# Kernel tuning notes

Hardware: AMD Instinct MI355X
Metric: run time of the kernel (lower is better)

The kernel has to match this reference:

```python
import jax, jax.numpy as jnp
import numpy as np

B, C, H, W = 32, 256, 64, 64
MIP, HID, OUT = 8, 256, 14  # mip = max(8, 256//32); per_eye=7 -> 2*7=14
MIN_Z, MAX_Z = 0.5, 1000.0


def _hswish(x):
    return x * jnp.clip(x + 3.0, 0.0, 6.0) / 6.0


def _bn(x, g, b, m, v, axis, eps=1e-5):
    sh = [1] * x.ndim
    sh[axis] = -1
    return (x - m.reshape(sh)) * (g.reshape(sh) / jnp.sqrt(v.reshape(sh) + eps)) + b.reshape(sh)


def _safe_norm(v, axis=-1, eps=1e-8):
    return v / (jnp.linalg.norm(v, axis=axis, keepdims=True) + eps)


def setup_inputs() -> dict:
    key = jax.random.key(0)
    ks = jax.random.split(key, 8)
    x = jax.random.normal(ks[0], (B, C, H, W), dtype=jnp.float32)
    K1 = jnp.array([[500.0, 0.0, 320.0], [0.0, 500.0, 240.0], [0.0, 0.0, 1.0]], jnp.float32)
    K = jnp.tile(K1[None], (B, 1, 1))
    iris_radius_cm = 0.6 * jnp.ones((B,), jnp.float32)
    s = 0.05
    return {
        'x': x, 'K': K, 'iris_radius_cm': iris_radius_cm,
        'ca_w1': s * jax.random.normal(ks[1], (MIP, C), jnp.float32),
        'ca_bn_g': jnp.ones((MIP,), jnp.float32), 'ca_bn_b': jnp.zeros((MIP,), jnp.float32),
        'ca_bn_m': jnp.zeros((MIP,), jnp.float32), 'ca_bn_v': jnp.ones((MIP,), jnp.float32),
        'ca_wh': s * jax.random.normal(ks[2], (C, MIP), jnp.float32),
        'ca_ww': s * jax.random.normal(ks[3], (C, MIP), jnp.float32),
        'fc1_w': s * jax.random.normal(ks[4], (HID, C), jnp.float32),
        'fc1_b': jnp.zeros((HID,), jnp.float32),
        'bn1_g': jnp.ones((HID,), jnp.float32), 'bn1_b': jnp.zeros((HID,), jnp.float32),
        'bn1_m': jnp.zeros((HID,), jnp.float32), 'bn1_v': jnp.ones((HID,), jnp.float32),
        'fc_out_w': s * jax.random.normal(ks[5], (OUT, HID), jnp.float32),
        'fc_out_b': jnp.zeros((OUT,), jnp.float32),
    }


def _forward(x, K, iris_radius_cm, ca_w1, ca_bn_g, ca_bn_b, ca_bn_m, ca_bn_v,
             ca_wh, ca_ww, fc1_w, fc1_b, bn1_g, bn1_b, bn1_m, bn1_v, fc_out_w, fc_out_b):
    b, c, h, w = x.shape
    # ---- CoordAtt ----
    xh = x.mean(axis=3)                      # [B,C,H]
    xw = x.mean(axis=2)                      # [B,C,W]
    y = jnp.concatenate([xh, xw], axis=2)    # [B,C,H+W]
    y = jnp.einsum('mc,bcl->bml', ca_w1, y)  # 1x1 conv -> [B,mip,H+W]
    y = _hswish(_bn(y, ca_bn_g, ca_bn_b, ca_bn_m, ca_bn_v, axis=1))
    a_h = jax.nn.sigmoid(jnp.einsum('cm,bmh->bch', ca_wh, y[:, :, :h]))[:, :, :, None]
    a_w = jax.nn.sigmoid(jnp.einsum('cm,bmw->bcw', ca_ww, y[:, :, h:]))[:, :, None, :]
    x = x * a_h * a_w
    # ---- pool + MLP head ----
    p = x.mean(axis=(2, 3))                                  # [B,C]
    hdd = jnp.maximum(_bn(p @ fc1_w.T + fc1_b, bn1_g, bn1_b, bn1_m, bn1_v, axis=1), 0.0)
    raw = hdd @ fc_out_w.T + fc_out_b                        # [B,14]
    t = raw.reshape(b, 2, 7)                                 # eyes L,R
    # ---- unpack per-eye ellipse ----
    cx, cy = t[..., 0], t[..., 1]
    ea = jax.nn.softplus(t[..., 2]) + 1e-6
    eb = jax.nn.softplus(t[..., 3]) + 1e-6
    ang = _safe_norm(t[..., 4:6])
    cth, sth = ang[..., 0], ang[..., 1]
    delta_cm = 0.3 * jnp.tanh(t[..., 6:7])                   # [B,2,1]
    ellipse = jnp.stack([cx, cy, ea, eb, cth, sth], axis=-1) # [B,2,6]
    # ---- ellipse -> conic C (pixel), then Cn = K^T C K ----
    theta = jnp.arctan2(sth, cth)
    ct, st = jnp.cos(theta), jnp.sin(theta)
    ia2, ib2 = 1.0 / (ea * ea), 1.0 / (eb * eb)
    A11 = ct * ct * ia2 + st * st * ib2
    A22 = st * st * ia2 + ct * ct * ib2
    A12 = ct * st * (ia2 - ib2)
    ax = A11 * cx + A12 * cy
    ay = A12 * cx + A22 * cy
    cAc = A11 * cx ** 2 + 2.0 * A12 * cx * cy + A22 * cy ** 2
    Cm = jnp.stack([jnp.stack([A11, A12, -ax], -1),
                    jnp.stack([A12, A22, -ay], -1),
                    jnp.stack([-ax, -ay, cAc - 1.0], -1)], -2)  # [B,2,3,3]
    Cn = jnp.einsum('bji,bejk,bkl->beil', K, Cm, K)             # [B,2,3,3]
    # ---- 2x2 solve + eigh on normalized conic ----
    A = Cn[..., :2, :2]
    u = Cn[..., :2, 2]
    mu = jnp.linalg.solve(A, -u[..., None])[..., 0]             # [B,2,2]
    evals, evecs = jnp.linalg.eigh(A)                           # ascending
    a_n = 1.0 / jnp.sqrt(jnp.maximum(evals[..., 0], 1e-12))
    b_n = 1.0 / jnp.sqrt(jnp.maximum(evals[..., 1], 1e-12))
    v = evecs[..., :, 0]
    theta_n = jnp.arctan2(v[..., 1], v[..., 0])                 # [B,2]
    # ---- lift to 3D pose + center ----
    a_n = jnp.maximum(a_n, 1e-6)
    R = iris_radius_cm[:, None]
    z = jnp.clip(R / a_n, MIN_Z, MAX_Z)[..., None]              # [B,2,1]
    ray = _safe_norm(jnp.stack([mu[..., 0], mu[..., 1], jnp.ones_like(mu[..., 0])], -1))
    iris_center = ray * z                                       # [B,2,3]
    tilt = jnp.arccos(jnp.clip(b_n / a_n, 0.0, 1.0))[..., None] # [B,2,1]
    axis3 = jnp.stack([jnp.cos(theta_n), jnp.sin(theta_n), jnp.zeros_like(theta_n)], -1)
    k = _safe_norm(axis3)
    z_ax = jnp.broadcast_to(jnp.array([0.0, 0.0, 1.0], x.dtype), k.shape)
    ctl, stl = jnp.cos(tilt), jnp.sin(tilt)
    kv = jnp.cross(k, z_ax)
    kdv = jnp.sum(k * z_ax, -1, keepdims=True)
    normal = _safe_norm(z_ax * ctl + kv * stl + k * (kdv * (1.0 - ctl)))
    pupil_center = iris_center + delta_cm * normal
    return ellipse, delta_cm, iris_center, normal, pupil_center, z


def reference(x, K, iris_radius_cm, ca_w1, ca_bn_g, ca_bn_b, ca_bn_m, ca_bn_v,
              ca_wh, ca_ww, fc1_w, fc1_b, bn1_g, bn1_b, bn1_m, bn1_v, fc_out_w, fc_out_b):
    return _forward(x, K, iris_radius_cm, ca_w1, ca_bn_g, ca_bn_b, ca_bn_m, ca_bn_v,
                    ca_wh, ca_ww, fc1_w, fc1_b, bn1_g, bn1_b, bn1_m, bn1_v, fc_out_w, fc_out_b)
```

## Files before the change

kernel.cpp:

```cpp
#include <hip/hip_runtime.h>
#include <math.h>

#define Bb 32
#define Cc 256
#define Hh 64
#define Ww 64
#define MIP 8
#define HID 256
#define NOUT 14

__global__ __launch_bounds__(256) void k1_sums(const float* __restrict__ x,
                                               float* __restrict__ S) {
    const int bc = blockIdx.x;
    const float4* xp = (const float4*)(x + (size_t)bc * (Hh * Ww));
    const int t = threadIdx.x;
    const int cw = t & 15;
    const int rb = t >> 4;
    __shared__ float rowpart[64][17];
    __shared__ float colpart[16][64];
    float4 v[4];
#pragma unroll
    for (int k = 0; k < 4; ++k) v[k] = xp[t + 256 * k];
    float c0 = 0.f, c1 = 0.f, c2 = 0.f, c3 = 0.f;
#pragma unroll
    for (int k = 0; k < 4; ++k) {
        rowpart[rb + 16 * k][cw] = v[k].x + v[k].y + v[k].z + v[k].w;
        c0 += v[k].x; c1 += v[k].y; c2 += v[k].z; c3 += v[k].w;
    }
    colpart[rb][cw * 4 + 0] = c0;
    colpart[rb][cw * 4 + 1] = c1;
    colpart[rb][cw * 4 + 2] = c2;
    colpart[rb][cw * 4 + 3] = c3;
    __syncthreads();
    float* out = S + (size_t)bc * 128;
    if (t < 64) {
        float s = 0.f;
#pragma unroll
        for (int i = 0; i < 16; ++i) s += rowpart[t][i];
        out[t] = s;
    } else if (t < 128) {
        const int w = t - 64;
        float s = 0.f;
#pragma unroll
        for (int g = 0; g < 16; ++g) s += colpart[g][w];
        out[64 + w] = s;
    }
}

__global__ __launch_bounds__(256) void k2_yact(const float* __restrict__ S,
                                               const float* __restrict__ w1,
                                               const float* __restrict__ bng,
                                               const float* __restrict__ bnb,
                                               const float* __restrict__ bnm,
                                               const float* __restrict__ bnv,
                                               float* __restrict__ yact) {
    const int b = blockIdx.x;
    const int t = threadIdx.x;
    const int half = __builtin_amdgcn_readfirstlane(t >> 7);
    const int l = t & 127;
    __shared__ float part[2][MIP][128];
    const float* Sp = S + (size_t)b * Cc * 128 + (size_t)half * 128 * 128 + l;
    const float* wp = w1 + half * 128;
    float a0 = 0.f, a1 = 0.f, a2 = 0.f, a3 = 0.f,
          a4 = 0.f, a5 = 0.f, a6 = 0.f, a7 = 0.f;
#pragma unroll 4
    for (int cc = 0; cc < 128; ++cc) {
        float s = Sp[(size_t)cc * 128];
        a0 += wp[0 * Cc + cc] * s;
        a1 += wp[1 * Cc + cc] * s;
        a2 += wp[2 * Cc + cc] * s;
        a3 += wp[3 * Cc + cc] * s;
        a4 += wp[4 * Cc + cc] * s;
        a5 += wp[5 * Cc + cc] * s;
        a6 += wp[6 * Cc + cc] * s;
        a7 += wp[7 * Cc + cc] * s;
    }
    part[half][0][l] = a0; part[half][1][l] = a1;
    part[half][2][l] = a2; part[half][3][l] = a3;
    part[half][4][l] = a4; part[half][5][l] = a5;
    part[half][6][l] = a6; part[half][7][l] = a7;
    __syncthreads();
    if (t < 128) {
#pragma unroll
        for (int m = 0; m < MIP; ++m) {
            float sum = (part[0][m][l] + part[1][m][l]) * (1.0f / 64.0f);
            float y = (sum - bnm[m]) * (bng[m] / sqrtf(bnv[m] + 1e-5f)) + bnb[m];
            float cl = fminf(fmaxf(y + 3.0f, 0.0f), 6.0f);
            yact[((size_t)b * MIP + m) * 128 + l] = y * cl * (1.0f / 6.0f);
        }
    }
}

__global__ __launch_bounds__(256) void k3_pool(const float* __restrict__ x,
                                               const float* __restrict__ yact,
                                               const float* __restrict__ wh,
                                               const float* __restrict__ ww,
                                               float* __restrict__ p) {
    const int bc = blockIdx.x;
    const int b = bc >> 8;
    const int c = bc & 255;
    const int t = threadIdx.x;
    __shared__ float ah[64], aw[64], red[4];
    if (t < 128) {
        const float* yb = yact + (size_t)b * MIP * 128;
        const float* wv = (t < 64) ? (wh + c * MIP) : (ww + c * MIP);
        float acc = 0.f;
#pragma unroll
        for (int m = 0; m < MIP; ++m) acc += wv[m] * yb[m * 128 + t];
        float s = 1.0f / (1.0f + expf(-acc));
        if (t < 64) ah[t] = s; else aw[t - 64] = s;
    }
    __syncthreads();
    const float4* xp = (const float4*)(x + (size_t)bc * (Hh * Ww));
    const int cw = t & 15, rb = t >> 4;
    float partial = 0.f;
#pragma unroll
    for (int k = 0; k < 4; ++k) {
        float4 v = xp[t + 256 * k];
        float rd = v.x * aw[cw * 4 + 0] + v.y * aw[cw * 4 + 1] +
                   v.z * aw[cw * 4 + 2] + v.w * aw[cw * 4 + 3];
        partial += ah[rb + 16 * k] * rd;
    }
#pragma unroll
    for (int off = 32; off > 0; off >>= 1) partial += __shfl_down(partial, off, 64);
    if ((t & 63) == 0) red[t >> 6] = partial;
    __syncthreads();
    if (t == 0) p[bc] = (red[0] + red[1] + red[2] + red[3]) * (1.0f / (float)(Hh * Ww));
}

__device__ inline double softplus_d(double xx) {
    return fmax(xx, 0.0) + log1p(exp(-fabs(xx)));
}

__global__ __launch_bounds__(256) void k4_head(
    const float* __restrict__ p,
    const float* __restrict__ fc1_w, const float* __restrict__ fc1_b,
    const float* __restrict__ bn1_g, const float* __restrict__ bn1_b,
    const float* __restrict__ bn1_m, const float* __restrict__ bn1_v,
    const float* __restrict__ fo_w, const float* __restrict__ fo_b,
    const float* __restrict__ Kmat, const float* __restrict__ iris_r,
    float* __restrict__ out) {
    const int b = blockIdx.x, t = threadIdx.x;
    __shared__ float pl[256], hdd[256], raw[16];
    __shared__ float part2[NOUT][16];
    pl[t] = p[b * 256 + t];
    __syncthreads();
    const float4* wrow = (const float4*)(fc1_w + (size_t)t * 256);
    float acc = fc1_b[t];
#pragma unroll 4
    for (int c4 = 0; c4 < 64; ++c4) {
        float4 w4 = wrow[c4];
        acc += w4.x * pl[c4 * 4] + w4.y * pl[c4 * 4 + 1] +
               w4.z * pl[c4 * 4 + 2] + w4.w * pl[c4 * 4 + 3];
    }
    float ybn = (acc - bn1_m[t]) * (bn1_g[t] / sqrtf(bn1_v[t] + 1e-5f)) + bn1_b[t];
    hdd[t] = fmaxf(ybn, 0.f);
    __syncthreads();
    if (t < NOUT * 16) {
        const int o = t >> 4, lane16 = t & 15;
        const float* wo = fo_w + o * HID + lane16;
        float a = 0.f;
#pragma unroll
        for (int j = 0; j < 16; ++j) a += wo[j * 16] * hdd[lane16 + j * 16];
        part2[o][lane16] = a;
    }
    __syncthreads();
    if (t < NOUT) {
        float a = fo_b[t];
#pragma unroll
        for (int i = 0; i < 16; ++i) a += part2[t][i];
        raw[t] = a;
    }
    __syncthreads();
    if (t < 2) {
        const int e = t;
        const float* tv = raw + e * 7;
        double t0 = tv[0], t1 = tv[1], t2 = tv[2], t3 = tv[3],
               t4 = tv[4], t5 = tv[5], t6 = tv[6];
        double cx = t0, cy = t1;
        double ea = softplus_d(t2) + 1e-6;
        double eb = softplus_d(t3) + 1e-6;
        double rr = sqrt(t4 * t4 + t5 * t5) + 1e-8;
        double cth = t4 / rr, sth = t5 / rr;
        double delta = 0.3 * tanh(t6);
        const int be = b * 2 + e;
        out[be * 6 + 0] = (float)cx;
        out[be * 6 + 1] = (float)cy;
        out[be * 6 + 2] = (float)ea;
        out[be * 6 + 3] = (float)eb;
        out[be * 6 + 4] = (float)cth;
        out[be * 6 + 5] = (float)sth;
        out[384 + be] = (float)delta;

        double ct = cth, st = sth;
        double ia2 = 1.0 / (ea * ea), ib2 = 1.0 / (eb * eb);
        double A11 = ct * ct * ia2 + st * st * ib2;
        double A22 = st * st * ia2 + ct * ct * ib2;
        double A12 = ct * st * (ia2 - ib2);
        double axp = A11 * cx + A12 * cy;
        double ayp = A12 * cx + A22 * cy;
        double cAc = A11 * cx * cx + 2.0 * A12 * cx * cy + A22 * cy * cy;
        double Cm[3][3] = {{A11, A12, -axp}, {A12, A22, -ayp}, {-axp, -ayp, cAc - 1.0}};
        double Kd[3][3];
        for (int i = 0; i < 3; ++i)
            for (int j = 0; j < 3; ++j) Kd[i][j] = (double)Kmat[b * 9 + i * 3 + j];
        double M[3][3], Cn[3][3];
        for (int j = 0; j < 3; ++j)
            for (int l = 0; l < 3; ++l) {
                double s = 0.0;
                for (int k = 0; k < 3; ++k) s += Cm[j][k] * Kd[k][l];
                M[j][l] = s;
            }
        for (int i = 0; i < 3; ++i)
            for (int l = 0; l < 3; ++l) {
                double s = 0.0;
                for (int j = 0; j < 3; ++j) s += Kd[j][i] * M[j][l];
                Cn[i][l] = s;
            }
        double Aa = Cn[0][0], Ab = Cn[1][0], Ac = Cn[1][1];
        double A01 = Cn[0][1];
        double u0 = Cn[0][2], u1 = Cn[1][2];
        double det = Aa * Ac - A01 * Ab;
        double mux = (A01 * u1 - Ac * u0) / det;
        double muy = (Ab * u0 - Aa * u1) / det;
        double sm = Aa + Ac, df = Aa - Ac;
        double adf = fabs(df);
        double tb = Ab + Ab, ab = fabs(tb);
        double acmx, acmn;
        if (fabs(Aa) > fabs(Ac)) { acmx = Aa; acmn = Ac; } else { acmx = Ac; acmn = Aa; }
        double rt;
        if (adf > ab)      rt = adf * sqrt(1.0 + (ab / adf) * (ab / adf));
        else if (adf < ab) rt = ab * sqrt(1.0 + (adf / ab) * (adf / ab));
        else               rt = ab * sqrt(2.0);
        double rt1, rt2; int sgn1;
        if (sm < 0.0)      { rt1 = 0.5 * (sm - rt); sgn1 = -1;
                             rt2 = (acmx / rt1) * acmn - (Ab / rt1) * Ab; }
        else if (sm > 0.0) { rt1 = 0.5 * (sm + rt); sgn1 = 1;
                             rt2 = (acmx / rt1) * acmn - (Ab / rt1) * Ab; }
        else               { rt1 = 0.5 * rt; rt2 = -0.5 * rt; sgn1 = 1; }
        double cs; int sgn2;
        if (df >= 0.0) { cs = df + rt; sgn2 = 1; } else { cs = df - rt; sgn2 = -1; }
        double acs = fabs(cs), cs1, sn1;
        if (acs > ab) {
            double ctv = -tb / cs;
            sn1 = 1.0 / sqrt(1.0 + ctv * ctv);
            cs1 = ctv * sn1;
        } else if (ab == 0.0) {
            cs1 = 1.0; sn1 = 0.0;
        } else {
            double tn = -cs / tb;
            cs1 = 1.0 / sqrt(1.0 + tn * tn);
            sn1 = tn * cs1;
        }
        if (sgn1 == sgn2) { double tmp = cs1; cs1 = -sn1; sn1 = tmp; }
        double lam0, lam1, vx, vy;
        if (rt2 < rt1) { lam0 = rt2; lam1 = rt1; vx = -sn1; vy = cs1; }
        else           { lam0 = rt1; lam1 = rt2; vx = cs1;  vy = sn1; }
        double a_n = 1.0 / sqrt(fmax(lam0, 1e-12));
        double b_n = 1.0 / sqrt(fmax(lam1, 1e-12));
        a_n = fmax(a_n, 1e-6);
        double Rir = (double)iris_r[b];
        double zz = fmin(fmax(Rir / a_n, 0.5), 1000.0);
        double rnorm = sqrt(mux * mux + muy * muy + 1.0) + 1e-8;
        double ic0 = (mux / rnorm) * zz, ic1 = (muy / rnorm) * zz, ic2 = (1.0 / rnorm) * zz;
        double a3x = vx, a3y = vy;
        double kn = sqrt(a3x * a3x + a3y * a3y) + 1e-8;
        double kx = a3x / kn, ky = a3y / kn;
        double rba = fmin(fmax(b_n / a_n, 0.0), 1.0);
        double ctl = rba, stl = sqrt(fmax(1.0 - rba * rba, 0.0));
        double nx = ky * stl, ny = -kx * stl, nz = ctl;
        double nn = sqrt(nx * nx + ny * ny + nz * nz) + 1e-8;
        nx /= nn; ny /= nn; nz /= nn;
        out[448 + be * 3 + 0] = (float)ic0;
        out[448 + be * 3 + 1] = (float)ic1;
        out[448 + be * 3 + 2] = (float)ic2;
        out[640 + be * 3 + 0] = (float)nx;
        out[640 + be * 3 + 1] = (float)ny;
        out[640 + be * 3 + 2] = (float)nz;
        out[832 + be * 3 + 0] = (float)(ic0 + delta * nx);
        out[832 + be * 3 + 1] = (float)(ic1 + delta * ny);
        out[832 + be * 3 + 2] = (float)(ic2 + delta * nz);
        out[1024 + be] = (float)zz;
    }
}

extern "C" void kernel_launch(void* const* d_in, const int* in_sizes, int n_in,
                              void* d_out, int out_size, void* d_ws, size_t ws_size,
                              hipStream_t stream) {
    const float* x     = (const float*)d_in[0];
    const float* Kmat  = (const float*)d_in[1];
    const float* iris  = (const float*)d_in[2];
    const float* ca_w1 = (const float*)d_in[3];
    const float* ca_g  = (const float*)d_in[4];
    const float* ca_b  = (const float*)d_in[5];
    const float* ca_m  = (const float*)d_in[6];
    const float* ca_v  = (const float*)d_in[7];
    const float* ca_wh = (const float*)d_in[8];
    const float* ca_ww = (const float*)d_in[9];
    const float* fc1_w = (const float*)d_in[10];
    const float* fc1_b = (const float*)d_in[11];
    const float* bn1_g = (const float*)d_in[12];
    const float* bn1_b = (const float*)d_in[13];
    const float* bn1_m = (const float*)d_in[14];
    const float* bn1_v = (const float*)d_in[15];
    const float* fo_w  = (const float*)d_in[16];
    const float* fo_b  = (const float*)d_in[17];

    float* ws   = (float*)d_ws;
    float* S    = ws;
    float* yact = S + (size_t)Bb * Cc * 128;
    float* p    = yact + (size_t)Bb * MIP * 128;

    k1_sums<<<Bb * Cc, 256, 0, stream>>>(x, S);
    k2_yact<<<Bb, 256, 0, stream>>>(S, ca_w1, ca_g, ca_b, ca_m, ca_v, yact);
    k3_pool<<<Bb * Cc, 256, 0, stream>>>(x, yact, ca_wh, ca_ww, p);
    k4_head<<<Bb, 256, 0, stream>>>(p, fc1_w, fc1_b, bn1_g, bn1_b, bn1_m, bn1_v,
                                    fo_w, fo_b, Kmat, iris, (float*)d_out);
}
```

Measured before the change: 267.8 us.

## Fuse per-batch reductions into producer kernels via last-block atomic counters

```diff
diff --git a/kernel.cpp b/kernel.cpp
--- a/kernel.cpp
+++ b/kernel.cpp
@@ -9,98 +9,120 @@
 #define HID 256
 #define NOUT 14
 
-__global__ __launch_bounds__(256) void k1_sums(const float* __restrict__ x,
-                                               float* __restrict__ S) {
+__global__ __launch_bounds__(256) void kA_sums_yact(
+    const float* __restrict__ x, float* __restrict__ S,
+    const float* __restrict__ w1,
+    const float* __restrict__ bng, const float* __restrict__ bnb,
+    const float* __restrict__ bnm, const float* __restrict__ bnv,
+    float* __restrict__ yact, unsigned int* __restrict__ cnt) {
     const int bc = blockIdx.x;
-    const float4* xp = (const float4*)(x + (size_t)bc * (Hh * Ww));
+    const int b = bc >> 8;
     const int t = threadIdx.x;
-    const int cw = t & 15;
-    const int rb = t >> 4;
     __shared__ float rowpart[64][17];
     __shared__ float colpart[16][64];
-    float4 v[4];
-#pragma unroll
-    for (int k = 0; k < 4; ++k) v[k] = xp[t + 256 * k];
-    float c0 = 0.f, c1 = 0.f, c2 = 0.f, c3 = 0.f;
-#pragma unroll
-    for (int k = 0; k < 4; ++k) {
-        rowpart[rb + 16 * k][cw] = v[k].x + v[k].y + v[k].z + v[k].w;
-        c0 += v[k].x; c1 += v[k].y; c2 += v[k].z; c3 += v[k].w;
-    }
-    colpart[rb][cw * 4 + 0] = c0;
-    colpart[rb][cw * 4 + 1] = c1;
-    colpart[rb][cw * 4 + 2] = c2;
-    colpart[rb][cw * 4 + 3] = c3;
-    __syncthreads();
-    float* out = S + (size_t)bc * 128;
-    if (t < 64) {
-        float s = 0.f;
-#pragma unroll
-        for (int i = 0; i < 16; ++i) s += rowpart[t][i];
-        out[t] = s;
-    } else if (t < 128) {
-        const int w = t - 64;
-        float s = 0.f;
-#pragma unroll
-        for (int g = 0; g < 16; ++g) s += colpart[g][w];
-        out[64 + w] = s;
+    __shared__ float part[2][MIP][128];
+    __shared__ int lasta;
+
+    {
+        const float4* xp = (const float4*)(x + (size_t)bc * (Hh * Ww));
+        const int cw = t & 15;
+        const int rb = t >> 4;
+        float4 v[4];
+#pragma unroll
+        for (int k = 0; k < 4; ++k) v[k] = xp[t + 256 * k];
+        float c0 = 0.f, c1 = 0.f, c2 = 0.f, c3 = 0.f;
+#pragma unroll
+        for (int k = 0; k < 4; ++k) {
+            rowpart[rb + 16 * k][cw] = v[k].x + v[k].y + v[k].z + v[k].w;
+            c0 += v[k].x; c1 += v[k].y; c2 += v[k].z; c3 += v[k].w;
+        }
+        colpart[rb][cw * 4 + 0] = c0;
+        colpart[rb][cw * 4 + 1] = c1;
+        colpart[rb][cw * 4 + 2] = c2;
+        colpart[rb][cw * 4 + 3] = c3;
+        __syncthreads();
+        float* out = S + (size_t)bc * 128;
+        if (t < 64) {
+            float s = 0.f;
+#pragma unroll
+            for (int i = 0; i < 16; ++i) s += rowpart[t][i];
+            out[t] = s;
+        } else if (t < 128) {
+            const int w = t - 64;
+            float s = 0.f;
+#pragma unroll
+            for (int g = 0; g < 16; ++g) s += colpart[g][w];
+            out[64 + w] = s;
+        }
+    }
+    __syncthreads();
+    if (t == 0) {
+        __threadfence();
+        lasta = (atomicAdd(&cnt[b], 1u) == (unsigned)(Cc - 1));
+    }
+    __syncthreads();
+    if (!lasta) return;
+    __threadfence();
+
+    {
+        const int half = __builtin_amdgcn_readfirstlane(t >> 7);
+        const int l = t & 127;
+        const float* Sp = S + (size_t)b * Cc * 128 + (size_t)half * 128 * 128 + l;
+        const float* wp = w1 + half * 128;
+        float a0 = 0.f, a1 = 0.f, a2 = 0.f, a3 = 0.f,
+              a4 = 0.f, a5 = 0.f, a6 = 0.f, a7 = 0.f;
+#pragma unroll 4
+        for (int cc = 0; cc < 128; ++cc) {
+            float s = Sp[(size_t)cc * 128];
+            a0 += wp[0 * Cc + cc] * s;
+            a1 += wp[1 * Cc + cc] * s;
+            a2 += wp[2 * Cc + cc] * s;
+            a3 += wp[3 * Cc + cc] * s;
+            a4 += wp[4 * Cc + cc] * s;
+            a5 += wp[5 * Cc + cc] * s;
+            a6 += wp[6 * Cc + cc] * s;
+            a7 += wp[7 * Cc + cc] * s;
+        }
+        part[half][0][l] = a0; part[half][1][l] = a1;
+        part[half][2][l] = a2; part[half][3][l] = a3;
+        part[half][4][l] = a4; part[half][5][l] = a5;
+        part[half][6][l] = a6; part[half][7][l] = a7;
+        __syncthreads();
+        if (t < 128) {
+#pragma unroll
+            for (int m = 0; m < MIP; ++m) {
+                float sum = (part[0][m][l] + part[1][m][l]) * (1.0f / 64.0f);
+                float y = (sum - bnm[m]) * (bng[m] / sqrtf(bnv[m] + 1e-5f)) + bnb[m];
+                float cl = fminf(fmaxf(y + 3.0f, 0.0f), 6.0f);
+                yact[((size_t)b * MIP + m) * 128 + l] = y * cl * (1.0f / 6.0f);
+            }
+        }
     }
 }
 
-__global__ __launch_bounds__(256) void k2_yact(const float* __restrict__ S,
-                                               const float* __restrict__ w1,
-                                               const float* __restrict__ bng,
-                                               const float* __restrict__ bnb,
-                                               const float* __restrict__ bnm,
-                                               const float* __restrict__ bnv,
-                                               float* __restrict__ yact) {
-    const int b = blockIdx.x;
-    const int t = threadIdx.x;
-    const int half = __builtin_amdgcn_readfirstlane(t >> 7);
-    const int l = t & 127;
-    __shared__ float part[2][MIP][128];
-    const float* Sp = S + (size_t)b * Cc * 128 + (size_t)half * 128 * 128 + l;
-    const float* wp = w1 + half * 128;
-    float a0 = 0.f, a1 = 0.f, a2 = 0.f, a3 = 0.f,
-          a4 = 0.f, a5 = 0.f, a6 = 0.f, a7 = 0.f;
-#pragma unroll 4
-    for (int cc = 0; cc < 128; ++cc) {
-        float s = Sp[(size_t)cc * 128];
-        a0 += wp[0 * Cc + cc] * s;
-        a1 += wp[1 * Cc + cc] * s;
-        a2 += wp[2 * Cc + cc] * s;
-        a3 += wp[3 * Cc + cc] * s;
-        a4 += wp[4 * Cc + cc] * s;
-        a5 += wp[5 * Cc + cc] * s;
-        a6 += wp[6 * Cc + cc] * s;
-        a7 += wp[7 * Cc + cc] * s;
-    }
-    part[half][0][l] = a0; part[half][1][l] = a1;
-    part[half][2][l] = a2; part[half][3][l] = a3;
-    part[half][4][l] = a4; part[half][5][l] = a5;
-    part[half][6][l] = a6; part[half][7][l] = a7;
-    __syncthreads();
-    if (t < 128) {
-#pragma unroll
-        for (int m = 0; m < MIP; ++m) {
-            float sum = (part[0][m][l] + part[1][m][l]) * (1.0f / 64.0f);
-            float y = (sum - bnm[m]) * (bng[m] / sqrtf(bnv[m] + 1e-5f)) + bnb[m];
-            float cl = fminf(fmaxf(y + 3.0f, 0.0f), 6.0f);
-            yact[((size_t)b * MIP + m) * 128 + l] = y * cl * (1.0f / 6.0f);
-        }
-    }
+__device__ inline double softplus_d(double xx) {
+    return fmax(xx, 0.0) + log1p(exp(-fabs(xx)));
 }
 
-__global__ __launch_bounds__(256) void k3_pool(const float* __restrict__ x,
-                                               const float* __restrict__ yact,
-                                               const float* __restrict__ wh,
-                                               const float* __restrict__ ww,
-                                               float* __restrict__ p) {
+__global__ __launch_bounds__(256) void kB_pool_head(
+    const float* __restrict__ x, const float* __restrict__ yact,
+    const float* __restrict__ wh, const float* __restrict__ ww,
+    float* __restrict__ p,
+    const float* __restrict__ fc1_w, const float* __restrict__ fc1_b,
+    const float* __restrict__ bn1_g, const float* __restrict__ bn1_b,
+    const float* __restrict__ bn1_m, const float* __restrict__ bn1_v,
+    const float* __restrict__ fo_w, const float* __restrict__ fo_b,
+    const float* __restrict__ Kmat, const float* __restrict__ iris_r,
+    float* __restrict__ out, unsigned int* __restrict__ cnt2) {
     const int bc = blockIdx.x;
     const int b = bc >> 8;
     const int c = bc & 255;
     const int t = threadIdx.x;
     __shared__ float ah[64], aw[64], red[4];
+    __shared__ float pl[256], hdd[256], raw[16];
+    __shared__ float part2[NOUT][16];
+    __shared__ int lastf;
+
     if (t < 128) {
         const float* yb = yact + (size_t)b * MIP * 128;
         const float* wv = (t < 64) ? (wh + c * MIP) : (ww + c * MIP);
@@ -111,50 +133,45 @@
         if (t < 64) ah[t] = s; else aw[t - 64] = s;
     }
     __syncthreads();
-    const float4* xp = (const float4*)(x + (size_t)bc * (Hh * Ww));
-    const int cw = t & 15, rb = t >> 4;
-    float partial = 0.f;
-#pragma unroll
-    for (int k = 0; k < 4; ++k) {
-        float4 v = xp[t + 256 * k];
-        float rd = v.x * aw[cw * 4 + 0] + v.y * aw[cw * 4 + 1] +
-                   v.z * aw[cw * 4 + 2] + v.w * aw[cw * 4 + 3];
-        partial += ah[rb + 16 * k] * rd;
-    }
-#pragma unroll
-    for (int off = 32; off > 0; off >>= 1) partial += __shfl_down(partial, off, 64);
-    if ((t & 63) == 0) red[t >> 6] = partial;
-    __syncthreads();
-    if (t == 0) p[bc] = (red[0] + red[1] + red[2] + red[3]) * (1.0f / (float)(Hh * Ww));
-}
-
-__device__ inline double softplus_d(double xx) {
-    return fmax(xx, 0.0) + log1p(exp(-fabs(xx)));
-}
-
-__global__ __launch_bounds__(256) void k4_head(
-    const float* __restrict__ p,
-    const float* __restrict__ fc1_w, const float* __restrict__ fc1_b,
-    const float* __restrict__ bn1_g, const float* __restrict__ bn1_b,
-    const float* __restrict__ bn1_m, const float* __restrict__ bn1_v,
-    const float* __restrict__ fo_w, const float* __restrict__ fo_b,
-    const float* __restrict__ Kmat, const float* __restrict__ iris_r,
-    float* __restrict__ out) {
-    const int b = blockIdx.x, t = threadIdx.x;
-    __shared__ float pl[256], hdd[256], raw[16];
-    __shared__ float part2[NOUT][16];
+    {
+        const float4* xp = (const float4*)(x + (size_t)bc * (Hh * Ww));
+        const int cw = t & 15, rb = t >> 4;
+        float partial = 0.f;
+#pragma unroll
+        for (int k = 0; k < 4; ++k) {
+            float4 v = xp[t + 256 * k];
+            float rd = v.x * aw[cw * 4 + 0] + v.y * aw[cw * 4 + 1] +
+                       v.z * aw[cw * 4 + 2] + v.w * aw[cw * 4 + 3];
+            partial += ah[rb + 16 * k] * rd;
+        }
+#pragma unroll
+        for (int off = 32; off > 0; off >>= 1) partial += __shfl_down(partial, off, 64);
+        if ((t & 63) == 0) red[t >> 6] = partial;
+    }
+    __syncthreads();
+    if (t == 0) {
+        p[bc] = (red[0] + red[1] + red[2] + red[3]) * (1.0f / (float)(Hh * Ww));
+        __threadfence();
+        lastf = (atomicAdd(&cnt2[b], 1u) == (unsigned)(Cc - 1));
+    }
+    __syncthreads();
+    if (!lastf) return;
+    __threadfence();
+
     pl[t] = p[b * 256 + t];
     __syncthreads();
-    const float4* wrow = (const float4*)(fc1_w + (size_t)t * 256);
-    float acc = fc1_b[t];
+    {
+        const float4* wrow = (const float4*)(fc1_w + (size_t)t * 256);
+        float acc = fc1_b[t];
 #pragma unroll 4
-    for (int c4 = 0; c4 < 64; ++c4) {
-        float4 w4 = wrow[c4];
-        acc += w4.x * pl[c4 * 4] + w4.y * pl[c4 * 4 + 1] +
-               w4.z * pl[c4 * 4 + 2] + w4.w * pl[c4 * 4 + 3];
-    }
-    float ybn = (acc - bn1_m[t]) * (bn1_g[t] / sqrtf(bn1_v[t] + 1e-5f)) + bn1_b[t];
-    hdd[t] = fmaxf(ybn, 0.f);
+        for (int c4 = 0; c4 < 64; ++c4) {
+            float4 w4 = wrow[c4];
+            acc += w4.x * pl[c4 * 4] + w4.y * pl[c4 * 4 + 1] +
+                   w4.z * pl[c4 * 4 + 2] + w4.w * pl[c4 * 4 + 3];
+        }
+        float ybn = (acc - bn1_m[t]) * (bn1_g[t] / sqrtf(bn1_v[t] + 1e-5f)) + bn1_b[t];
+        hdd[t] = fmaxf(ybn, 0.f);
+    }
     __syncthreads();
     if (t < NOUT * 16) {
         const int o = t >> 4, lane16 = t & 15;
@@ -310,10 +327,15 @@
     float* S    = ws;
     float* yact = S + (size_t)Bb * Cc * 128;
     float* p    = yact + (size_t)Bb * MIP * 128;
-
-    k1_sums<<<Bb * Cc, 256, 0, stream>>>(x, S);
-    k2_yact<<<Bb, 256, 0, stream>>>(S, ca_w1, ca_g, ca_b, ca_m, ca_v, yact);
-    k3_pool<<<Bb * Cc, 256, 0, stream>>>(x, yact, ca_wh, ca_ww, p);
-    k4_head<<<Bb, 256, 0, stream>>>(p, fc1_w, fc1_b, bn1_g, bn1_b, bn1_m, bn1_v,
-                                    fo_w, fo_b, Kmat, iris, (float*)d_out);
+    unsigned int* cnt = (unsigned int*)(p + (size_t)Bb * Cc);
+
+    hipMemsetAsync(cnt, 0, 2 * Bb * sizeof(unsigned int), stream);
+
+    kA_sums_yact<<<Bb * Cc, 256, 0, stream>>>(x, S, ca_w1, ca_g, ca_b, ca_m,
+                                              ca_v, yact, cnt);
+    kB_pool_head<<<Bb * Cc, 256, 0, stream>>>(x, yact, ca_wh, ca_ww, p,
+                                              fc1_w, fc1_b, bn1_g, bn1_b,
+                                              bn1_m, bn1_v, fo_w, fo_b,
+                                              Kmat, iris, (float*)d_out,
+                                              cnt + Bb);
 }
```

Result: slower. 936.7 us (+249.8%).
